# Optimization experiments

Measured on AMD Instinct MI355X. Metric: run time of the kernel, lower is better.

Reference implementation:

```python
import jax, jax.numpy as jnp
import numpy as np

N = 100_000   # nodes
E = 3_200_000 # edges
G = 128       # graphs in batch
H = 32        # hidden_dim
PI = float(np.pi)


def setup_inputs() -> dict:
    key = jax.random.key(0)
    ks = jax.random.split(key, 18)
    p = lambda k, s: (jax.random.normal(k, s, dtype=jnp.float32) * 0.1)
    x = jax.random.normal(ks[0], (N, 1), dtype=jnp.float32)
    edge_index = jax.random.randint(ks[1], (2, E), 0, N, dtype=jnp.int32)
    batch = jnp.sort(jax.random.randint(ks[2], (N,), 0, G, dtype=jnp.int32))
    return dict(
        x=x, edge_index=edge_index, batch=batch,
        W1=p(ks[3], (1, H)),  b1=jnp.zeros((H,), jnp.float32),
        W2=p(ks[4], (H, H)),  b2=jnp.zeros((H,), jnp.float32),
        W3=p(ks[5], (H, H)),  b3=jnp.zeros((H,), jnp.float32),
        Wt1=p(ks[6], (H, 32)), bt1=jnp.zeros((32,), jnp.float32),
        Wt2=p(ks[7], (32, 1)), bt2=jnp.zeros((1,), jnp.float32),
        Wg1=p(ks[8], (H, 32)), bg1=jnp.zeros((32,), jnp.float32),
        Wg2=p(ks[9], (32, 2)), bg2=jnp.zeros((2,), jnp.float32),
    )


def _gcn_norm(edge_index):
    # PyG GCNConv default: add self-loops, symmetric normalization.
    loop = jnp.arange(N, dtype=edge_index.dtype)
    src = jnp.concatenate([edge_index[0], loop])
    dst = jnp.concatenate([edge_index[1], loop])
    deg = jax.ops.segment_sum(jnp.ones_like(dst, dtype=jnp.float32), dst, num_segments=N)
    dinv = jnp.where(deg > 0, jax.lax.rsqrt(jnp.maximum(deg, 1.0)), 0.0)
    norm = dinv[src] * dinv[dst]  # [E+N]
    return src, dst, norm


def _gcn_conv(x, W, b, src, dst, norm):
    h = x @ W                                  # [N, out]
    msg = h[src] * norm[:, None]               # gather + scale  [E+N, out]
    return jax.ops.segment_sum(msg, dst, num_segments=N) + b


def _forward(x, W1, b1, W2, b2, W3, b3, Wt1, bt1, Wt2, bt2, Wg1, bg1, Wg2, bg2,
             edge_index, batch):
    src, dst, norm = _gcn_norm(edge_index)
    x = jax.nn.relu(_gcn_conv(x, W1, b1, src, dst, norm))
    x = jax.nn.relu(_gcn_conv(x, W2, b2, src, dst, norm))
    h = jax.nn.relu(_gcn_conv(x, W3, b3, src, dst, norm))
    # theta head per node
    theta = PI * jax.nn.sigmoid(jax.nn.relu(h @ Wt1 + bt1) @ Wt2 + bt2)[:, 0]  # [N]
    # global mean pool per graph
    counts = jax.ops.segment_sum(jnp.ones((N,), jnp.float32), batch, num_segments=G)
    gsum = jax.ops.segment_sum(h, batch, num_segments=G)
    gemb = gsum / jnp.maximum(counts, 1.0)[:, None]                            # [G, H]
    beta_gamma = 2.0 * PI * jax.nn.sigmoid(jax.nn.relu(gemb @ Wg1 + bg1) @ Wg2 + bg2)  # [G, 2]
    return theta, beta_gamma


def reference(x, edge_index, batch, W1, b1, W2, b2, W3, b3,
              Wt1, bt1, Wt2, bt2, Wg1, bg1, Wg2, bg2):
    return _forward(x, W1, b1, W2, b2, W3, b3, Wt1, bt1, Wt2, bt2,
                    Wg1, bg1, Wg2, bg2, edge_index, batch)
```

## Files before the change

kernel.cpp:

```cpp
#include <hip/hip_runtime.h>
#include <hip/hip_bf16.h>

#define PI_F 3.14159265358979323846f
#define NBLK 256
#define BSH 8
#define BSZ 256
#define SCAP 10240
#define SLDS 3072

static inline size_t align256(size_t x) { return (x + 255) & ~size_t(255); }

typedef float v2f __attribute__((ext_vector_type(2)));
typedef unsigned uvec4 __attribute__((ext_vector_type(4)));

__device__ __forceinline__ unsigned bfpack(float a, float b) {
    unsigned lo = (__float_as_uint(a) + 0x8000u) >> 16;
    unsigned hi = (__float_as_uint(b) + 0x8000u) & 0xFFFF0000u;
    return lo | hi;
}

__device__ __forceinline__ void f8acc(uint2 q, float rs, float acc[8]) {
    v2f l0 = __builtin_amdgcn_cvt_pk_f32_fp8(q.x, false);
    v2f h0 = __builtin_amdgcn_cvt_pk_f32_fp8(q.x, true);
    v2f l1 = __builtin_amdgcn_cvt_pk_f32_fp8(q.y, false);
    v2f h1 = __builtin_amdgcn_cvt_pk_f32_fp8(q.y, true);
    acc[0] += rs * l0.x; acc[1] += rs * l0.y; acc[2] += rs * h0.x; acc[3] += rs * h0.y;
    acc[4] += rs * l1.x; acc[5] += rs * l1.y; acc[6] += rs * h1.x; acc[7] += rs * h1.y;
}


__global__ void __launch_bounds__(1024) count_kernel(
                             const int* __restrict__ dst, int* __restrict__ C,
                             int E, int CHUNK, int NB2) {
    extern __shared__ int hist[];
    for (int i = threadIdx.x; i < NB2; i += 1024) hist[i] = 0;
    __syncthreads();
    int s0 = blockIdx.x * CHUNK, s1 = min(s0 + CHUNK, E);
    for (int e = s0 + threadIdx.x; e < s1; e += 1024)
        atomicAdd(&hist[dst[e] >> BSH], 1);
    __syncthreads();
    for (int i = threadIdx.x; i < NB2; i += 1024)
        C[(size_t)blockIdx.x * NB2 + i] = hist[i];
}

__global__ void scan_blocks_kernel(int* __restrict__ C, int* __restrict__ colsum, int NB2) {
    __shared__ int s[256];
    int k = blockIdx.x;
    int b = threadIdx.x;
    int v = C[(size_t)b * NB2 + k];
    s[b] = v;
    __syncthreads();
    for (int off = 1; off < 256; off <<= 1) {
        int w = (b >= off) ? s[b - off] : 0;
        __syncthreads();
        s[b] += w;
        __syncthreads();
    }
    C[(size_t)b * NB2 + k] = s[b] - v;
    if (b == 255) colsum[k] = s[255];
}

__global__ void scan_totals_kernel(const int* __restrict__ colsum, int* __restrict__ bbase,
                                   int NB2, int E) {
    __shared__ int s[256];
    __shared__ int running;
    if (threadIdx.x == 0) running = 0;
    __syncthreads();
    for (int base = 0; base < NB2; base += 256) {
        int i = base + threadIdx.x;
        int v = (i < NB2) ? colsum[i] : 0;
        s[threadIdx.x] = v;
        __syncthreads();
        for (int off = 1; off < 256; off <<= 1) {
            int w = (threadIdx.x >= (unsigned)off) ? s[threadIdx.x - off] : 0;
            __syncthreads();
            s[threadIdx.x] += w;
            __syncthreads();
        }
        if (i < NB2) bbase[i] = running + s[threadIdx.x] - v;
        __syncthreads();
        if (threadIdx.x == 255) running += s[255];
        __syncthreads();
    }
    if (threadIdx.x == 0) bbase[NB2] = E;
}

__global__ void __launch_bounds__(1024) scatter_kernel(
                               const int* __restrict__ src, const int* __restrict__ dst,
                               const int* __restrict__ C, const int* __restrict__ bbase,
                               unsigned* __restrict__ bkt_data, int E, int CHUNK, int NB2) {
    extern __shared__ int ofs[];
    for (int i = threadIdx.x; i < NB2; i += 1024)
        ofs[i] = bbase[i] + C[(size_t)blockIdx.x * NB2 + i];
    __syncthreads();
    int s0 = blockIdx.x * CHUNK, s1 = min(s0 + CHUNK, E);
    for (int e = s0 + threadIdx.x; e < s1; e += 1024) {
        int d = dst[e];
        int p = atomicAdd(&ofs[d >> BSH], 1);
        bkt_data[p] = ((unsigned)(d & (BSZ - 1)) << 17) | (unsigned)src[e];
    }
}

__global__ void __launch_bounds__(512) csr_build_kernel(
                                 const unsigned* __restrict__ bkt_data, const int* __restrict__ bbase,
                                 const float* __restrict__ x,
                                 unsigned* __restrict__ csr, int* __restrict__ e_start,
                                 float* __restrict__ dinv, float* __restrict__ xd,
                                 int N, int NB2) {
    __shared__ unsigned sdata[SCAP];
    __shared__ int hist[256];
    __shared__ int scn[256];
    __shared__ int bump[256];
    int tid = threadIdx.x;
    int b = blockIdx.x;
    int g0 = bbase[b], g1 = bbase[b + 1];
    int cnt = g1 - g0;
    bool fits = (cnt <= SCAP);
    if (tid < 256) hist[tid] = 0;
    __syncthreads();
    for (int i = tid; i < cnt; i += 512) {
        unsigned pk = bkt_data[g0 + i];
        if (fits) sdata[i] = pk;
        atomicAdd(&hist[pk >> 17], 1);
    }
    __syncthreads();
    int orig = (tid < 256) ? hist[tid] : 0;
    if (tid < 256) scn[tid] = orig;
    __syncthreads();
    for (int off = 1; off < 256; off <<= 1) {
        int w = (tid >= off && tid < 256) ? scn[tid - off] : 0;
        __syncthreads();
        if (tid < 256) scn[tid] += w;
        __syncthreads();
    }
    if (tid < 256) {
        int excl = scn[tid] - orig;
        bump[tid] = g0 + excl;
        int node = b * BSZ + tid;
        if (node < N) {
            float dv = rsqrtf((float)(orig + 1));
            dinv[node] = dv;
            xd[node] = x[node] * dv;
            e_start[node] = g0 + excl;
        }
    }
    if (b == NB2 - 1 && tid == 0) e_start[N] = g1;
    __syncthreads();
    for (int i = tid; i < cnt; i += 512) {
        unsigned pk = fits ? sdata[i] : bkt_data[g0 + i];
        int p = atomicAdd(&bump[pk >> 17], 1);
        csr[p] = pk & 0x1FFFFu;
    }
}


__device__ __forceinline__ void mm32_8(const float* __restrict__ sW, const float vr[8],
                                       int sub, int lane, float o[8]) {
    const float4* sW4 = (const float4*)sW;
    int base = lane & ~3;
#pragma unroll
    for (int r = 0; r < 4; r++) {
#pragma unroll
        for (int i = 0; i < 8; i++) {
            float vk = __shfl(vr[i], base | r, 64);
            int k = r * 8 + i;
            float4 w0 = sW4[k * 8 + sub * 2];
            float4 w1 = sW4[k * 8 + sub * 2 + 1];
            o[0] += vk * w0.x; o[1] += vk * w0.y; o[2] += vk * w0.z; o[3] += vk * w0.w;
            o[4] += vk * w1.x; o[5] += vk * w1.y; o[6] += vk * w1.z; o[7] += vk * w1.w;
        }
    }
}

__device__ __forceinline__ void store_f8(unsigned char* __restrict__ u8, float* __restrict__ uscale,
                                         int d, int sub, const float o[8]) {
    float am = 0.f;
#pragma unroll
    for (int i = 0; i < 8; i++) am = fmaxf(am, fabsf(o[i]));
    am = fmaxf(am, __shfl_xor(am, 1, 64));
    am = fmaxf(am, __shfl_xor(am, 2, 64));
    float rm = fmaxf(am, 1e-20f);
    float sc = 128.f / rm;
    unsigned w0 = 0, w1 = 0;
    w0 = __builtin_amdgcn_cvt_pk_fp8_f32(o[0] * sc, o[1] * sc, w0, false);
    w0 = __builtin_amdgcn_cvt_pk_fp8_f32(o[2] * sc, o[3] * sc, w0, true);
    w1 = __builtin_amdgcn_cvt_pk_fp8_f32(o[4] * sc, o[5] * sc, w1, false);
    w1 = __builtin_amdgcn_cvt_pk_fp8_f32(o[6] * sc, o[7] * sc, w1, true);
    uint2 st; st.x = w0; st.y = w1;
    ((uint2*)u8)[(size_t)d * 4 + sub] = st;
    if (sub == 0) uscale[d] = rm * (1.f / 128.f);
}

__device__ __forceinline__ bool stage_csr(const unsigned* __restrict__ csr,
                                          const int* __restrict__ e_start,
                                          int d0, int dEnd, int* sidx, int& E0) {
    E0 = e_start[d0];
    int E1 = e_start[dEnd];
    int m = E1 - E0;
    bool fits = (m <= SLDS);
    if (fits) {
        for (int i = threadIdx.x; i < m; i += 256)
            sidx[i] = (int)__builtin_nontemporal_load(&csr[E0 + i]);
    }
    __syncthreads();
    return fits;
}

__global__ void __launch_bounds__(256) agg1_kernel(
                            const float* __restrict__ xd, const int* __restrict__ e_start,
                            const unsigned* __restrict__ csr, const float* __restrict__ dinv,
                            const float* __restrict__ W1, const float* __restrict__ b1,
                            const float* __restrict__ W2,
                            unsigned char* __restrict__ u8o, float* __restrict__ uso, int n) {
    __shared__ float sW2[1024];
    __shared__ float sW1[32], sb1[32];
    __shared__ int sidx[SLDS];
    for (int i = threadIdx.x; i < 1024; i += 256) sW2[i] = W2[i];
    if (threadIdx.x < 32) { sW1[threadIdx.x] = W1[threadIdx.x]; sb1[threadIdx.x] = b1[threadIdx.x]; }
    int d0 = blockIdx.x * 64;
    int dEnd = min(d0 + 64, n);
    int E0;
    bool fits = stage_csr(csr, e_start, d0, dEnd, sidx, E0);
    int d = d0 + (threadIdx.x >> 2), sub = threadIdx.x & 3;
    int lane = threadIdx.x & 63;
    if (d >= n) return;
    int e0 = e_start[d];
    int cnt = e_start[d + 1] - e0;
    int l0 = e0 - E0;
    float s = 0.f;
    int j = sub;
    if (fits) {
        for (; j < cnt; j += 4) s += xd[sidx[l0 + j]];
    } else {
        for (; j < cnt; j += 4) s += xd[(int)csr[e0 + j]];
    }
    s += __shfl_xor(s, 1, 64);
    s += __shfl_xor(s, 2, 64);
    float dv = dinv[d];
    float tt = dv * (s + xd[d]);
    float vr[8];
#pragma unroll
    for (int i = 0; i < 8; i++) vr[i] = fmaxf(tt * sW1[sub * 8 + i] + sb1[sub * 8 + i], 0.f);
    float o[8];
#pragma unroll
    for (int i = 0; i < 8; i++) o[i] = 0.f;
    mm32_8(sW2, vr, sub, lane, o);
#pragma unroll
    for (int i = 0; i < 8; i++) o[i] *= dv;
    store_f8(u8o, uso, d, sub, o);
}

__device__ __forceinline__ void gather_f8(const unsigned char* __restrict__ u8,
                                          const float* __restrict__ uscale,
                                          const int* __restrict__ sidx, bool fits,
                                          const unsigned* __restrict__ csr,
                                          int e0, int l0, int cnt, int d, int sub, float acc[8]) {
#pragma unroll
    for (int i = 0; i < 8; i++) acc[i] = 0.f;
    const uint2* rows = (const uint2*)u8;
    int j = 0;
    if (fits) {
        for (; j + 8 <= cnt; j += 8) {
            int id[8];
#pragma unroll
            for (int k = 0; k < 8; k++) id[k] = sidx[l0 + j + k];
            float rs[8];
#pragma unroll
            for (int k = 0; k < 8; k++) rs[k] = uscale[id[k]];
            uint2 q[8];
#pragma unroll
            for (int k = 0; k < 8; k++) q[k] = rows[(size_t)id[k] * 4 + sub];
#pragma unroll
            for (int k = 0; k < 8; k++) f8acc(q[k], rs[k], acc);
        }
        for (; j < cnt; j++) {
            int i0 = sidx[l0 + j];
            f8acc(rows[(size_t)i0 * 4 + sub], uscale[i0], acc);
        }
    } else {
        for (; j + 4 <= cnt; j += 4) {
            int i0 = (int)csr[e0 + j],     i1 = (int)csr[e0 + j + 1];
            int i2 = (int)csr[e0 + j + 2], i3 = (int)csr[e0 + j + 3];
            float r0 = uscale[i0], r1 = uscale[i1], r2 = uscale[i2], r3 = uscale[i3];
            uint2 q0 = rows[(size_t)i0 * 4 + sub];
            uint2 q1 = rows[(size_t)i1 * 4 + sub];
            uint2 q2 = rows[(size_t)i2 * 4 + sub];
            uint2 q3 = rows[(size_t)i3 * 4 + sub];
            f8acc(q0, r0, acc); f8acc(q1, r1, acc); f8acc(q2, r2, acc); f8acc(q3, r3, acc);
        }
        for (; j < cnt; j++) {
            int i0 = (int)csr[e0 + j];
            f8acc(rows[(size_t)i0 * 4 + sub], uscale[i0], acc);
        }
    }
    f8acc(rows[(size_t)d * 4 + sub], uscale[d], acc);
}

__global__ void __launch_bounds__(256) agg2_kernel(
                            const unsigned char* __restrict__ u8, const float* __restrict__ uscale,
                            const int* __restrict__ e_start, const unsigned* __restrict__ csr,
                            const float* __restrict__ dinv, const float* __restrict__ bias,
                            const float* __restrict__ W,
                            unsigned char* __restrict__ o8, float* __restrict__ oscale, int n) {
    __shared__ float sW[1024];
    __shared__ float sb[32];
    __shared__ int sidx[SLDS];
    for (int i = threadIdx.x; i < 1024; i += 256) sW[i] = W[i];
    if (threadIdx.x < 32) sb[threadIdx.x] = bias[threadIdx.x];
    int d0 = blockIdx.x * 64;
    int dEnd = min(d0 + 64, n);
    int E0;
    bool fits = stage_csr(csr, e_start, d0, dEnd, sidx, E0);
    int d = d0 + (threadIdx.x >> 2), sub = threadIdx.x & 3;
    int lane = threadIdx.x & 63;
    if (d >= n) return;
    int e0 = e_start[d];
    int cnt = e_start[d + 1] - e0;
    float acc[8];
    gather_f8(u8, uscale, sidx, fits, csr, e0, e0 - E0, cnt, d, sub, acc);
    float dv = dinv[d];
    float vr[8];
#pragma unroll
    for (int i = 0; i < 8; i++) vr[i] = fmaxf(dv * acc[i] + sb[sub * 8 + i], 0.f);
    float o[8];
#pragma unroll
    for (int i = 0; i < 8; i++) o[i] = 0.f;
    mm32_8(sW, vr, sub, lane, o);
#pragma unroll
    for (int i = 0; i < 8; i++) o[i] *= dv;
    store_f8(o8, oscale, d, sub, o);
}

__global__ void __launch_bounds__(256) agg3_kernel(
                            const unsigned char* __restrict__ u8, const float* __restrict__ uscale,
                            const int* __restrict__ e_start, const unsigned* __restrict__ csr,
                            const float* __restrict__ dinv, const float* __restrict__ bias,
                            const float* __restrict__ Wt1, const float* __restrict__ bt1,
                            const float* __restrict__ Wt2, const float* __restrict__ bt2,
                            unsigned short* __restrict__ hb, float* __restrict__ theta, int n) {
    __shared__ float sW[1024];
    __shared__ float sb[32], sbt[32], sw2[32];
    __shared__ int sidx[SLDS];
    for (int i = threadIdx.x; i < 1024; i += 256) sW[i] = Wt1[i];
    if (threadIdx.x < 32) {
        sb[threadIdx.x] = bias[threadIdx.x];
        sbt[threadIdx.x] = bt1[threadIdx.x];
        sw2[threadIdx.x] = Wt2[threadIdx.x];
    }
    int d0 = blockIdx.x * 64;
    int dEnd = min(d0 + 64, n);
    int E0;
    bool fits = stage_csr(csr, e_start, d0, dEnd, sidx, E0);
    int d = d0 + (threadIdx.x >> 2), sub = threadIdx.x & 3;
    int lane = threadIdx.x & 63;
    if (d >= n) return;
    int e0 = e_start[d];
    int cnt = e_start[d + 1] - e0;
    float acc[8];
    gather_f8(u8, uscale, sidx, fits, csr, e0, e0 - E0, cnt, d, sub, acc);
    float dv = dinv[d];
    float vr[8];
#pragma unroll
    for (int i = 0; i < 8; i++) vr[i] = fmaxf(dv * acc[i] + sb[sub * 8 + i], 0.f);
    uvec4 st;
    st.x = bfpack(vr[0], vr[1]);
    st.y = bfpack(vr[2], vr[3]);
    st.z = bfpack(vr[4], vr[5]);
    st.w = bfpack(vr[6], vr[7]);
    __builtin_nontemporal_store(st, (uvec4*)hb + (size_t)d * 4 + sub);
    float o[8];
#pragma unroll
    for (int i = 0; i < 8; i++) o[i] = 0.f;
    mm32_8(sW, vr, sub, lane, o);
    float tl = 0.f;
#pragma unroll
    for (int i = 0; i < 8; i++)
        tl += fmaxf(o[i] + sbt[sub * 8 + i], 0.f) * sw2[sub * 8 + i];
    tl += __shfl_xor(tl, 1, 64);
    tl += __shfl_xor(tl, 2, 64);
    if (sub == 0) __builtin_nontemporal_store(PI_F / (1.f + __expf(-(tl + bt2[0]))), theta + d);
}


__global__ void gb_kernel(const int* __restrict__ batch, int* __restrict__ gstart,
                          int n, int G) {
    int i = blockIdx.x * 256 + threadIdx.x;
    if (i >= n) return;
    int g = batch[i];
    if (i == 0) {
        for (int gg = 0; gg <= g; gg++) gstart[gg] = 0;
    } else {
        int gp = batch[i - 1];
        for (int gg = gp + 1; gg <= g; gg++) gstart[gg] = i;
    }
    if (i == n - 1) {
        for (int gg = g + 1; gg <= G; gg++) gstart[gg] = n;
    }
}

__global__ void __launch_bounds__(512) bg_kernel(
                          const unsigned short* __restrict__ hb, const int* __restrict__ gstart,
                          const float* __restrict__ Wg1, const float* __restrict__ bg1v,
                          const float* __restrict__ Wg2, const float* __restrict__ bg2v,
                          float* __restrict__ out, int G) {
    __shared__ float sW[1024];
    __shared__ float part[8][32];
    for (int i = threadIdx.x; i < 1024; i += 512) sW[i] = Wg1[i];
    int g = blockIdx.x;
    int s = gstart[g], e = gstart[g + 1];
    int w = threadIdx.x >> 6;
    int lane = threadIdx.x & 63;
    int f = lane & 31, h = lane >> 5;
    float a = 0.f;
    for (int i = s + (w << 1) + h; i < e; i += 16)
        a += __uint_as_float((unsigned)hb[((size_t)i << 5) + f] << 16);
    a += __shfl_xor(a, 32, 64);
    if (h == 0) part[w][f] = a;
    __syncthreads();
    if (w == 0) {
        float hv = 0.f;
#pragma unroll
        for (int p = 0; p < 8; p++) hv += part[p][f];
        hv /= fmaxf((float)(e - s), 1.f);
        int base = lane & 32;
        float acc = bg1v[f];
#pragma unroll
        for (int k = 0; k < 32; k++) acc += __shfl(hv, base | k, 64) * sW[k * 32 + f];
        acc = fmaxf(acc, 0.f);
        float p0 = acc * Wg2[f * 2 + 0];
        float p1 = acc * Wg2[f * 2 + 1];
#pragma unroll
        for (int m = 1; m < 32; m <<= 1) {
            p0 += __shfl_xor(p0, m, 64);
            p1 += __shfl_xor(p1, m, 64);
        }
        if (lane == 0) {
            out[g * 2 + 0] = 2.f * PI_F / (1.f + __expf(-(p0 + bg2v[0])));
            out[g * 2 + 1] = 2.f * PI_F / (1.f + __expf(-(p1 + bg2v[1])));
        }
    }
}


extern "C" void kernel_launch(void* const* d_in, const int* in_sizes, int n_in,
                              void* d_out, int out_size, void* d_ws, size_t ws_size,
                              hipStream_t stream) {
    const float* x   = (const float*)d_in[0];
    const int*   ei  = (const int*)d_in[1];
    const int* batch = (const int*)d_in[2];
    const float* W1  = (const float*)d_in[3];
    const float* b1  = (const float*)d_in[4];
    const float* W2  = (const float*)d_in[5];
    const float* b2  = (const float*)d_in[6];
    const float* W3  = (const float*)d_in[7];
    const float* b3  = (const float*)d_in[8];
    const float* Wt1 = (const float*)d_in[9];
    const float* bt1 = (const float*)d_in[10];
    const float* Wt2 = (const float*)d_in[11];
    const float* bt2 = (const float*)d_in[12];
    const float* Wg1 = (const float*)d_in[13];
    const float* bg1 = (const float*)d_in[14];
    const float* Wg2 = (const float*)d_in[15];
    const float* bg2 = (const float*)d_in[16];

    const int N = in_sizes[0];
    const int E = in_sizes[1] / 2;
    const int G = 128;
    const int* src = ei;
    const int* dst = ei + E;
    float* theta_out = (float*)d_out;
    float* bg_out = (float*)d_out + N;

    const int NB2 = (N + BSZ - 1) >> BSH;
    const int CHUNK = (E + NBLK - 1) / NBLK;

    char* w = (char*)d_ws;
    auto alloc = [&](size_t bytes) -> char* { char* p = w; w += align256(bytes); return p; };
    int*      C        = (int*)alloc((size_t)NBLK * NB2 * 4);
    int*      colsum   = (int*)alloc((size_t)NB2 * 4);
    int*      bbase    = (int*)alloc((size_t)(NB2 + 1) * 4);
    unsigned* bkt_data = (unsigned*)alloc((size_t)E * 4);
    unsigned* csr      = (unsigned*)alloc((size_t)E * 4);
    int*      e_start  = (int*)alloc((size_t)(N + 1) * 4);
    float*    dinv     = (float*)alloc((size_t)N * 4);
    float*    xd       = (float*)alloc((size_t)N * 4);
    unsigned char* u2  = (unsigned char*)alloc((size_t)N * 32);
    float*    us2      = (float*)alloc((size_t)N * 4);
    unsigned char* u3  = (unsigned char*)alloc((size_t)N * 32);
    float*    us3      = (float*)alloc((size_t)N * 4);
    unsigned short* hb = (unsigned short*)alloc((size_t)N * 64);
    int*      gstart   = (int*)alloc((size_t)(G + 1) * 4);

    size_t ldsB = (size_t)NB2 * 4;
    count_kernel<<<NBLK, 1024, ldsB, stream>>>(dst, C, E, CHUNK, NB2);
    scan_blocks_kernel<<<NB2, 256, 0, stream>>>(C, colsum, NB2);
    scan_totals_kernel<<<1, 256, 0, stream>>>(colsum, bbase, NB2, E);
    scatter_kernel<<<NBLK, 1024, ldsB, stream>>>(src, dst, C, bbase, bkt_data, E, CHUNK, NB2);
    csr_build_kernel<<<NB2, 512, 0, stream>>>(bkt_data, bbase, x, csr, e_start, dinv, xd, N, NB2);
    gb_kernel<<<(N + 255) / 256, 256, 0, stream>>>(batch, gstart, N, G);

    unsigned gridQ = (unsigned)(((size_t)N * 4 + 255) / 256);

    agg1_kernel<<<gridQ, 256, 0, stream>>>(xd, e_start, csr, dinv, W1, b1, W2, u2, us2, N);
    agg2_kernel<<<gridQ, 256, 0, stream>>>(u2, us2, e_start, csr, dinv, b2, W3, u3, us3, N);
    agg3_kernel<<<gridQ, 256, 0, stream>>>(u3, us3, e_start, csr, dinv, b3,
                                           Wt1, bt1, Wt2, bt2, hb, theta_out, N);

    bg_kernel<<<G, 512, 0, stream>>>(hb, gstart, Wg1, bg1, Wg2, bg2, bg_out, G);
}
```

Measured before the change: 282.2 us.

## Fold graph-boundary kernel into scan, use nontemporal gathers, shrink unroll

The separate gb_kernel launch is removed and its graph-start computation moved into scan_blocks_kernel, which has NB2*256 threads (NB2 = ceil(N/256) buckets), enough to cover all nodes. Feature-row, scale and xd gathers in the aggregation kernels now use nontemporal loads, and the LDS-staged gather loop drops from 8-way to 4-way unrolling. This saves one launch and is meant to reduce cache pollution, but nontemporal hints on randomly reused rows could hurt cache hit rates, and less unrolling gives less memory-level parallelism. The bg_kernel output guard also changes from lane==0 to f==0.

```diff
diff --git a/kernel.cpp b/kernel.cpp
--- a/kernel.cpp
+++ b/kernel.cpp
@@ -11,6 +11,7 @@
 static inline size_t align256(size_t x) { return (x + 255) & ~size_t(255); }
 
 typedef float v2f __attribute__((ext_vector_type(2)));
+typedef unsigned uvec2 __attribute__((ext_vector_type(2)));
 typedef unsigned uvec4 __attribute__((ext_vector_type(4)));
 
 __device__ __forceinline__ unsigned bfpack(float a, float b) {
@@ -19,7 +20,7 @@
     return lo | hi;
 }
 
-__device__ __forceinline__ void f8acc(uint2 q, float rs, float acc[8]) {
+__device__ __forceinline__ void f8acc(uvec2 q, float rs, float acc[8]) {
     v2f l0 = __builtin_amdgcn_cvt_pk_f32_fp8(q.x, false);
     v2f h0 = __builtin_amdgcn_cvt_pk_f32_fp8(q.x, true);
     v2f l1 = __builtin_amdgcn_cvt_pk_f32_fp8(q.y, false);
@@ -43,7 +44,9 @@
         C[(size_t)blockIdx.x * NB2 + i] = hist[i];
 }
 
-__global__ void scan_blocks_kernel(int* __restrict__ C, int* __restrict__ colsum, int NB2) {
+__global__ void scan_blocks_kernel(int* __restrict__ C, int* __restrict__ colsum, int NB2,
+                                   const int* __restrict__ batch, int* __restrict__ gstart,
+                                   int n, int G) {
     __shared__ int s[256];
     int k = blockIdx.x;
     int b = threadIdx.x;
@@ -58,6 +61,19 @@
     }
     C[(size_t)b * NB2 + k] = s[b] - v;
     if (b == 255) colsum[k] = s[255];
+    int i = k * 256 + b;
+    if (i < n) {
+        int g = batch[i];
+        if (i == 0) {
+            for (int gg = 0; gg <= g; gg++) gstart[gg] = 0;
+        } else {
+            int gp = batch[i - 1];
+            for (int gg = gp + 1; gg <= g; gg++) gstart[gg] = i;
+        }
+        if (i == n - 1) {
+            for (int gg = g + 1; gg <= G; gg++) gstart[gg] = n;
+        }
+    }
 }
 
 __global__ void scan_totals_kernel(const int* __restrict__ colsum, int* __restrict__ bbase,
@@ -186,8 +202,8 @@
     w0 = __builtin_amdgcn_cvt_pk_fp8_f32(o[2] * sc, o[3] * sc, w0, true);
     w1 = __builtin_amdgcn_cvt_pk_fp8_f32(o[4] * sc, o[5] * sc, w1, false);
     w1 = __builtin_amdgcn_cvt_pk_fp8_f32(o[6] * sc, o[7] * sc, w1, true);
-    uint2 st; st.x = w0; st.y = w1;
-    ((uint2*)u8)[(size_t)d * 4 + sub] = st;
+    uvec2 st; st.x = w0; st.y = w1;
+    ((uvec2*)u8)[(size_t)d * 4 + sub] = st;
     if (sub == 0) uscale[d] = rm * (1.f / 128.f);
 }
 
@@ -230,9 +246,9 @@
     float s = 0.f;
     int j = sub;
     if (fits) {
-        for (; j < cnt; j += 4) s += xd[sidx[l0 + j]];
+        for (; j < cnt; j += 4) s += __builtin_nontemporal_load(&xd[sidx[l0 + j]]);
     } else {
-        for (; j < cnt; j += 4) s += xd[(int)csr[e0 + j]];
+        for (; j < cnt; j += 4) s += __builtin_nontemporal_load(&xd[(int)csr[e0 + j]]);
     }
     s += __shfl_xor(s, 1, 64);
     s += __shfl_xor(s, 2, 64);
@@ -257,43 +273,51 @@
                                           int e0, int l0, int cnt, int d, int sub, float acc[8]) {
 #pragma unroll
     for (int i = 0; i < 8; i++) acc[i] = 0.f;
-    const uint2* rows = (const uint2*)u8;
+    const uvec2* rows = (const uvec2*)u8;
     int j = 0;
     if (fits) {
-        for (; j + 8 <= cnt; j += 8) {
-            int id[8];
-#pragma unroll
-            for (int k = 0; k < 8; k++) id[k] = sidx[l0 + j + k];
-            float rs[8];
-#pragma unroll
-            for (int k = 0; k < 8; k++) rs[k] = uscale[id[k]];
-            uint2 q[8];
-#pragma unroll
-            for (int k = 0; k < 8; k++) q[k] = rows[(size_t)id[k] * 4 + sub];
-#pragma unroll
-            for (int k = 0; k < 8; k++) f8acc(q[k], rs[k], acc);
+        for (; j + 4 <= cnt; j += 4) {
+            int i0 = sidx[l0 + j],     i1 = sidx[l0 + j + 1];
+            int i2 = sidx[l0 + j + 2], i3 = sidx[l0 + j + 3];
+            float r0 = __builtin_nontemporal_load(&uscale[i0]);
+            float r1 = __builtin_nontemporal_load(&uscale[i1]);
+            float r2 = __builtin_nontemporal_load(&uscale[i2]);
+            float r3 = __builtin_nontemporal_load(&uscale[i3]);
+            uvec2 q0 = __builtin_nontemporal_load(rows + (size_t)i0 * 4 + sub);
+            uvec2 q1 = __builtin_nontemporal_load(rows + (size_t)i1 * 4 + sub);
+            uvec2 q2 = __builtin_nontemporal_load(rows + (size_t)i2 * 4 + sub);
+            uvec2 q3 = __builtin_nontemporal_load(rows + (size_t)i3 * 4 + sub);
+            f8acc(q0, r0, acc); f8acc(q1, r1, acc); f8acc(q2, r2, acc); f8acc(q3, r3, acc);
         }
         for (; j < cnt; j++) {
             int i0 = sidx[l0 + j];
-            f8acc(rows[(size_t)i0 * 4 + sub], uscale[i0], acc);
+            float r0 = __builtin_nontemporal_load(&uscale[i0]);
+            uvec2 q0 = __builtin_nontemporal_load(rows + (size_t)i0 * 4 + sub);
+            f8acc(q0, r0, acc);
         }
     } else {
         for (; j + 4 <= cnt; j += 4) {
             int i0 = (int)csr[e0 + j],     i1 = (int)csr[e0 + j + 1];
             int i2 = (int)csr[e0 + j + 2], i3 = (int)csr[e0 + j + 3];
-            float r0 = uscale[i0], r1 = uscale[i1], r2 = uscale[i2], r3 = uscale[i3];
-            uint2 q0 = rows[(size_t)i0 * 4 + sub];
-            uint2 q1 = rows[(size_t)i1 * 4 + sub];
-            uint2 q2 = rows[(size_t)i2 * 4 + sub];
-            uint2 q3 = rows[(size_t)i3 * 4 + sub];
+            float r0 = __builtin_nontemporal_load(&uscale[i0]);
+            float r1 = __builtin_nontemporal_load(&uscale[i1]);
+            float r2 = __builtin_nontemporal_load(&uscale[i2]);
+            float r3 = __builtin_nontemporal_load(&uscale[i3]);
+            uvec2 q0 = __builtin_nontemporal_load(rows + (size_t)i0 * 4 + sub);
+            uvec2 q1 = __builtin_nontemporal_load(rows + (size_t)i1 * 4 + sub);
+            uvec2 q2 = __builtin_nontemporal_load(rows + (size_t)i2 * 4 + sub);
+            uvec2 q3 = __builtin_nontemporal_load(rows + (size_t)i3 * 4 + sub);
             f8acc(q0, r0, acc); f8acc(q1, r1, acc); f8acc(q2, r2, acc); f8acc(q3, r3, acc);
         }
         for (; j < cnt; j++) {
             int i0 = (int)csr[e0 + j];
-            f8acc(rows[(size_t)i0 * 4 + sub], uscale[i0], acc);
-        }
-    }
-    f8acc(rows[(size_t)d * 4 + sub], uscale[d], acc);
+            float r0 = __builtin_nontemporal_load(&uscale[i0]);
+            uvec2 q0 = __builtin_nontemporal_load(rows + (size_t)i0 * 4 + sub);
+            f8acc(q0, r0, acc);
+        }
+    }
+    uvec2 qs = rows[(size_t)d * 4 + sub];
+    f8acc(qs, uscale[d], acc);
 }
 
 __global__ void __launch_bounds__(256) agg2_kernel(
@@ -382,22 +406,6 @@
 }
 
 
-__global__ void gb_kernel(const int* __restrict__ batch, int* __restrict__ gstart,
-                          int n, int G) {
-    int i = blockIdx.x * 256 + threadIdx.x;
-    if (i >= n) return;
-    int g = batch[i];
-    if (i == 0) {
-        for (int gg = 0; gg <= g; gg++) gstart[gg] = 0;
-    } else {
-        int gp = batch[i - 1];
-        for (int gg = gp + 1; gg <= g; gg++) gstart[gg] = i;
-    }
-    if (i == n - 1) {
-        for (int gg = g + 1; gg <= G; gg++) gstart[gg] = n;
-    }
-}
-
 __global__ void __launch_bounds__(512) bg_kernel(
                           const unsigned short* __restrict__ hb, const int* __restrict__ gstart,
                           const float* __restrict__ Wg1, const float* __restrict__ bg1v,
@@ -434,7 +442,7 @@
             p0 += __shfl_xor(p0, m, 64);
             p1 += __shfl_xor(p1, m, 64);
         }
-        if (lane == 0) {
+        if (f == 0) {
             out[g * 2 + 0] = 2.f * PI_F / (1.f + __expf(-(p0 + bg2v[0])));
             out[g * 2 + 1] = 2.f * PI_F / (1.f + __expf(-(p1 + bg2v[1])));
         }
@@ -493,11 +501,10 @@
 
     size_t ldsB = (size_t)NB2 * 4;
     count_kernel<<<NBLK, 1024, ldsB, stream>>>(dst, C, E, CHUNK, NB2);
-    scan_blocks_kernel<<<NB2, 256, 0, stream>>>(C, colsum, NB2);
+    scan_blocks_kernel<<<NB2, 256, 0, stream>>>(C, colsum, NB2, batch, gstart, N, G);
     scan_totals_kernel<<<1, 256, 0, stream>>>(colsum, bbase, NB2, E);
     scatter_kernel<<<NBLK, 1024, ldsB, stream>>>(src, dst, C, bbase, bkt_data, E, CHUNK, NB2);
     csr_build_kernel<<<NB2, 512, 0, stream>>>(bkt_data, bbase, x, csr, e_start, dinv, xd, N, NB2);
-    gb_kernel<<<(N + 255) / 256, 256, 0, stream>>>(batch, gstart, N, G);
 
     unsigned gridQ = (unsigned)(((size_t)N * 4 + 255) / 256);
 
```

Measured after the change: 376.5 us. +33.4%, slower.
